# Optimization experiments

Measured on AMD Instinct MI355X. Metric: run time of the kernel, lower is better.

Reference implementation:

```python
import jax, jax.numpy as jnp
import numpy as np

N = 4_000_000   # points at level d
SIDE = 1024     # coordinate range per axis
HALF = SIDE // 2  # parent coord range


def setup_inputs() -> dict:
    key = jax.random.key(0)
    k1, k2 = jax.random.split(key)
    xyz = jax.random.randint(k1, (N, 3), 0, SIDE, dtype=jnp.int32)
    b = (jnp.arange(N, dtype=jnp.int32) % 4)[:, None]  # 4 batches
    coords = jnp.concatenate([b, xyz], axis=1)          # (N,4): [b,x,y,z]
    kernel = jnp.ones((8,), dtype=jnp.float32)          # frozen all-ones 2x2x2 conv weights
    return {"coords": coords, "kernel": kernel}


def _fog(coords, kernel):
    # pos(): occupancy code 2**(x%2 + 2*y%2 + 4*z%2)
    bits = coords[:, 1:4] & 1                       # (N,3)
    off = bits[:, 0] + 2 * bits[:, 1] + 4 * bits[:, 2]  # (N,) child offset in 2x2x2 window
    pos = jnp.exp2(off.astype(jnp.float32))         # (N,) code in {1,2,4,...,128}
    contrib = pos * kernel[off]                     # per-offset conv weight (all ones)
    # stride-2 conv: parent voxel = floor(xyz/2); linearize (b,z,y,x) into a key
    parent = coords[:, 1:4] >> 1                    # (N,3)
    keys = (((coords[:, 0].astype(jnp.int64) * HALF + parent[:, 2]) * HALF
             + parent[:, 1]) * HALF + parent[:, 0])
    ukeys, inv = jnp.unique(keys, return_inverse=True, size=N, fill_value=-1)
    feats = jax.ops.segment_sum(contrib, inv, num_segments=N)[:, None]  # (N,1)
    # decode padded unique keys back to coords; pad slots -> -1
    px = (ukeys % HALF).astype(jnp.int32)
    py = ((ukeys // HALF) % HALF).astype(jnp.int32)
    pz = ((ukeys // (HALF * HALF)) % HALF).astype(jnp.int32)
    pb = (ukeys // (HALF * HALF * HALF)).astype(jnp.int32)
    valid = (ukeys >= 0)[:, None]
    coords_out = jnp.where(valid, jnp.stack([pb, px, py, pz], axis=1), -1)
    return coords_out, feats


def reference(coords, kernel):
    return _fog(coords, kernel)
```

## Files before the change

kernel.cpp:

```cpp
#include <hip/hip_runtime.h>
#include <stdint.h>

typedef unsigned int u32;
typedef unsigned long long u64;

#define LBITS  14
#define LMASK  ((1u << LBITS) - 1u)
#define NBUCK  (1u << (29 - LBITS))
#define BWORDS (1u << (LBITS - 5))
#define WPL    (BWORDS / 64)
#define WOPAD  (BWORDS + BWORDS / 32)
#define FCAP   192
#define BPB    4
#define TILE_A 4096
#define RPT    (TILE_A / 256)
#define CCAP   16384
#define P2T    1024
#define RPT2U  (CCAP / P2T)
#define RECV   4

__device__ __forceinline__ u32 woidx(u32 w) { return w + (w >> 5); }

__device__ __forceinline__ void wsync() {
    asm volatile("s_waitcnt lgkmcnt(0)" ::: "memory");
}

__device__ __forceinline__ u32 make_key(int4 c) {
    return ((((u32)c.x * 512u + ((u32)c.w >> 1)) * 512u + ((u32)c.z >> 1)) * 512u)
           + ((u32)c.y >> 1);
}

__global__ void zero1(u32* __restrict__ p, u32 g) {
    u32 i = blockIdx.x * 256u + threadIdx.x;
    if (i < g) p[i] = 0u;
}

__global__ void __launch_bounds__(256) part1f(const int4* __restrict__ coords,
        u32* __restrict__ ccur, u32* __restrict__ tmp, int n) {
    __shared__ u32 stage[TILE_A];
    __shared__ u32 lcur[256];
    __shared__ u32 gb[256];
    __shared__ u32 wtot[4];
    u32 t = threadIdx.x, wave = t >> 6, lane = t & 63u;
    u32 base = blockIdx.x * TILE_A;
    u32 m = min((u32)TILE_A, (u32)n - base);
    lcur[t] = 0u;
    __syncthreads();
    u32 recv[RPT];
    #pragma unroll
    for (int k = 0; k < RPT; ++k) {
        u32 j = (u32)k * 256u + t;
        if (j < m) {
            int4 c = coords[base + j];
            u32 key = make_key(c);
            u32 off = ((u32)c.y & 1u) | (((u32)c.z & 1u) << 1) | (((u32)c.w & 1u) << 2);
            u32 rec = (key << 3) | off;
            recv[k] = rec;
            atomicAdd(&lcur[rec >> 24], 1u);
        }
    }
    __syncthreads();
    u32 v = lcur[t];
    u32 incl = v;
    #pragma unroll
    for (int d = 1; d < 64; d <<= 1) {
        u32 x = __shfl_up(incl, d);
        if ((int)lane >= d) incl += x;
    }
    if (lane == 63u) wtot[wave] = incl;
    __syncthreads();
    u32 off = (wave > 0u ? wtot[0] : 0u) + (wave > 1u ? wtot[1] : 0u)
            + (wave > 2u ? wtot[2] : 0u);
    u32 excl = off + incl - v;
    u32 gbase = atomicAdd(&ccur[t * 16u], v);
    lcur[t] = excl;
    gb[t] = (t << 14) + gbase - excl;
    __syncthreads();
    #pragma unroll
    for (int k = 0; k < RPT; ++k) {
        u32 j = (u32)k * 256u + t;
        if (j < m) {
            u32 rec = recv[k];
            u32 pos = atomicAdd(&lcur[rec >> 24], 1u);
            stage[pos] = rec;
        }
    }
    __syncthreads();
    for (u32 j = t; j < m; j += 256u) {
        u32 rec = stage[j];
        tmp[gb[rec >> 24] + j] = rec;
    }
}

__global__ void __launch_bounds__(P2T) part2u(u32* __restrict__ tmp,
        const u32* __restrict__ ccur, u32* __restrict__ cstart,
        u32* __restrict__ bcnt, u32* __restrict__ lexc, u32* __restrict__ utot) {
    __shared__ u32 stage[CCAP];
    __shared__ u32 h[4][128];
    __shared__ u32 lstart[128];
    __shared__ u32 lcur[128];
    __shared__ u32 cnts[128];
    __shared__ u32 ucl[128];
    __shared__ u32 wtot[2];
    __shared__ u32 bm[16][WOPAD];
    u32 t = threadIdx.x, wave = t >> 6, lane = t & 63u;
    u32 c = blockIdx.x;
    u32 base = c << 14;
    u32 L = ccur[c * 16u];
    if (t < 512u) h[t >> 7][t & 127u] = 0u;
    __syncthreads();
    u32 recv[RPT2U];
    u32 hrep = wave & 3u;
    #pragma unroll
    for (int k = 0; k < RPT2U; ++k) {
        u32 j = (u32)k * P2T + t;
        if (j < L) {
            u32 rec = tmp[base + j];
            recv[k] = rec;
            atomicAdd(&h[hrep][(rec >> 17) & 127u], 1u);
        }
    }
    __syncthreads();
    u32 v = 0, incl = 0;
    if (t < 128u) {
        v = h[0][t] + h[1][t] + h[2][t] + h[3][t];
        incl = v;
        #pragma unroll
        for (int d = 1; d < 64; d <<= 1) {
            u32 x = __shfl_up(incl, d);
            if ((int)lane >= d) incl += x;
        }
        if (lane == 63u) wtot[t >> 6] = incl;
    }
    __syncthreads();
    if (t < 128u) {
        u32 off = (t >= 64u) ? wtot[0] : 0u;
        u32 excl = off + incl - v;
        lstart[t] = excl;
        lcur[t] = excl;
        cnts[t] = v;
        u32 bucket = (c << 7) | t;
        cstart[bucket] = base + excl;
        bcnt[bucket] = v;
    }
    __syncthreads();
    #pragma unroll
    for (int k = 0; k < RPT2U; ++k) {
        u32 j = (u32)k * P2T + t;
        if (j < L) {
            u32 rec = recv[k];
            u32 pos = atomicAdd(&lcur[(rec >> 17) & 127u], 1u);
            stage[pos] = rec;
        }
    }
    __syncthreads();
    for (u32 j = t; j < L; j += P2T) tmp[base + j] = stage[j];
    u32* B = bm[wave];
    for (u32 bi = 0; bi < 8u; ++bi) {
        u32 b = wave * 8u + bi;
        #pragma unroll
        for (int j = 0; j < WPL; ++j) B[woidx(lane * WPL + j)] = 0u;
        wsync();
        u32 s0 = lstart[b], cnt = cnts[b];
        for (u32 i = s0 + lane; i < s0 + cnt; i += 64u) {
            u32 lk = (stage[i] >> 3) & LMASK;
            atomicOr(&B[woidx(lk >> 5)], 1u << (lk & 31u));
        }
        wsync();
        u32 sum = 0;
        #pragma unroll
        for (int j = 0; j < WPL; ++j) sum += __popc(B[woidx(lane * WPL + j)]);
        #pragma unroll
        for (int d = 1; d < 64; d <<= 1) sum += __shfl_xor(sum, d);
        if (lane == 0u) ucl[b] = sum;
        wsync();
    }
    __syncthreads();
    u32 uv = 0, incl2 = 0;
    if (t < 128u) {
        uv = ucl[t];
        incl2 = uv;
        #pragma unroll
        for (int d = 1; d < 64; d <<= 1) {
            u32 x = __shfl_up(incl2, d);
            if ((int)lane >= d) incl2 += x;
        }
        if (lane == 63u) wtot[t >> 6] = incl2;
    }
    __syncthreads();
    if (t < 128u) {
        u32 off = (t >= 64u) ? wtot[0] : 0u;
        lexc[(c << 7) | t] = off + incl2 - uv;
        if (t == 127u) utot[c] = wtot[0] + incl2;
    }
}

__global__ void __launch_bounds__(256) pass_emit(const u32* __restrict__ buckrec,
        const u32* __restrict__ cstart, const u32* __restrict__ bcnt,
        const u32* __restrict__ lexc, const u32* __restrict__ utot,
        const float* __restrict__ kern, float4* __restrict__ rows,
        float* __restrict__ feats, int n) {
    __shared__ u32 bm[BPB][WOPAD];
    __shared__ u32 wofW[BPB][BWORDS];
    __shared__ float fl[BPB][FCAP];
    __shared__ float ksc[BPB][8];
    u32 wave = threadIdx.x >> 6, lane = threadIdx.x & 63u;
    u32 bucket = blockIdx.x * BPB + wave;
    u32* B = bm[wave];
    u32* W = wofW[wave];
    float* F = fl[wave];
    #pragma unroll
    for (int j = 0; j < WPL; ++j) B[woidx(lane * WPL + j)] = 0u;
    #pragma unroll
    for (u32 j = lane; j < FCAP; j += 64u) F[j] = 0.f;
    if (lane < 8u) ksc[wave][lane] = (float)(1u << lane) * kern[lane];
    wsync();
    u32 start = cstart[bucket];
    u32 cnt = bcnt[bucket];
    u32 recv[RECV];
    #pragma unroll
    for (int k = 0; k < RECV; ++k) {
        u32 idx = (u32)k * 64u + lane;
        if (idx < cnt) {
            u32 rec = buckrec[start + idx];
            recv[k] = rec;
            u32 lk = (rec >> 3) & LMASK;
            atomicOr(&B[woidx(lk >> 5)], 1u << (lk & 31u));
        }
    }
    u32 c = bucket >> 7;
    u32 cb = 0, Uall = 0;
    #pragma unroll
    for (int k = 0; k < 4; ++k) {
        u32 j = (u32)k * 64u + lane;
        u32 uv = utot[j];
        Uall += uv;
        cb += (j < c) ? uv : 0u;
    }
    #pragma unroll
    for (int d = 1; d < 64; d <<= 1) {
        cb += __shfl_xor(cb, d);
        Uall += __shfl_xor(Uall, d);
    }
    wsync();
    u32 wv[WPL]; u32 pc[WPL]; u32 sum = 0;
    #pragma unroll
    for (int j = 0; j < WPL; ++j) {
        wv[j] = B[woidx(lane * WPL + j)];
        pc[j] = __popc(wv[j]);
        sum += pc[j];
    }
    u32 incl = sum;
    #pragma unroll
    for (int d = 1; d < 64; d <<= 1) {
        u32 tt = __shfl_up(incl, d);
        if ((int)lane >= d) incl += tt;
    }
    u32 lex = incl - sum;
    u32 uc = __shfl(incl, 63);
    {
        u32 r = lex;
        #pragma unroll
        for (int j = 0; j < WPL; ++j) { W[((u32)j << 6) | lane] = r; r += pc[j]; }
    }
    wsync();
    u32 base = cb + lexc[bucket];
    bool lds_ok = (uc <= FCAP);
    if (!lds_ok) {
        for (u32 j = lane; j < uc; j += 64u) feats[base + j] = 0.f;
        asm volatile("s_waitcnt vmcnt(0)" ::: "memory");
    }
    #pragma unroll
    for (int k = 0; k < RECV; ++k) {
        u32 idx = (u32)k * 64u + lane;
        if (idx < cnt) {
            u32 rec = recv[k];
            float contrib = ksc[wave][rec & 7u];
            u32 lk = (rec >> 3) & LMASK;
            u32 w = lk >> 5, bit = lk & 31u;
            u32 r = W[((w & 7u) << 6) | (w >> 3)]
                  + __popc(B[woidx(w)] & ((1u << bit) - 1u));
            if (lds_ok) atomicAdd(&F[r], contrib);
            else        atomicAdd(&feats[base + r], contrib);
        }
    }
    wsync();
    u32 rank = base + lex;
    u32 keyhi = bucket << LBITS;
    #pragma unroll
    for (int j = 0; j < WPL; ++j) {
        u32 bits = wv[j];
        u32 kb = keyhi | ((lane * (u32)WPL + (u32)j) << 5);
        while (bits) {
            u32 tz = __builtin_ctz(bits);
            bits &= bits - 1u;
            u32 key = kb | tz;
            rows[rank++] = make_float4((float)(key >> 27), (float)(key & 511u),
                                       (float)((key >> 9) & 511u),
                                       (float)((key >> 18) & 511u));
        }
    }
    if (lds_ok) {
        for (u32 j = lane; j < uc; j += 64u) feats[base + j] = F[j];
    }
    u32 len = (u32)n - Uall;
    u32 per = (len + (u32)NBUCK - 1u) / (u32)NBUCK;
    u32 ps = Uall + bucket * per;
    u32 pe = min(ps + per, (u32)n);
    for (u32 i = ps + lane; i < pe; i += 64u) {
        rows[i] = make_float4(-1.f, -1.f, -1.f, -1.f);
        feats[i] = 0.f;
    }
}

extern "C" void kernel_launch(void* const* d_in, const int* in_sizes, int n_in,
                              void* d_out, int out_size, void* d_ws, size_t ws_size,
                              hipStream_t stream) {
    const int n = in_sizes[0] / 4;
    const int4* coords = (const int4*)d_in[0];
    const float* kern  = (const float*)d_in[1];
    const u32 NT = ((u32)n + TILE_A - 1) / TILE_A;

    u32* wsp = (u32*)d_ws;
    u32* tmp     = wsp;
    u32* ccur    = tmp + 256 * CCAP;
    u32* cstart  = ccur + 256 * 16;
    u32* bcnt    = cstart + NBUCK;
    u32* lexc    = bcnt + NBUCK;
    u32* utot    = lexc + NBUCK;

    float4* rows  = (float4*)d_out;
    float*  feats = (float*)((char*)d_out + (size_t)n * 16);

    zero1<<<16, 256, 0, stream>>>(ccur, 256 * 16);
    part1f<<<NT, 256, 0, stream>>>(coords, ccur, tmp, n);
    part2u<<<256, P2T, 0, stream>>>(tmp, ccur, cstart, bcnt, lexc, utot);
    pass_emit<<<NBUCK / BPB, 256, 0, stream>>>(tmp, cstart, bcnt, lexc, utot,
                                               kern, rows, feats, n);
}
```

Baseline: 193.4 us.

## Compute unique ranks in part2u and emit coalesced rows from LDS

part2u already builds a per-bucket occupancy bitmap to count unique keys. It now also prefix-sums that bitmap, computes each record's rank within its bucket, and packs the rank into the record's upper bits before writing the records back. pass_emit no longer rebuilds the bitmap and rank tables: it scatters contributions and keys by rank into LDS, then writes rows and feats with contiguous lane-strided stores instead of per-lane serial bit-walking writes. The global-atomic fallback for buckets with more uniques than FCAP is removed, with FCAP raised to 224. Correctness therefore relies on no bucket exceeding that many unique parents.

```diff
diff --git a/kernel.cpp b/kernel.cpp
--- a/kernel.cpp
+++ b/kernel.cpp
@@ -10,14 +10,13 @@
 #define BWORDS (1u << (LBITS - 5))
 #define WPL    (BWORDS / 64)
 #define WOPAD  (BWORDS + BWORDS / 32)
-#define FCAP   192
+#define FCAP   224
 #define BPB    4
 #define TILE_A 4096
 #define RPT    (TILE_A / 256)
 #define CCAP   16384
 #define P2T    1024
 #define RPT2U  (CCAP / P2T)
-#define RECV   4
 
 __device__ __forceinline__ u32 woidx(u32 w) { return w + (w >> 5); }
 
@@ -94,7 +93,8 @@
 
 __global__ void __launch_bounds__(P2T) part2u(u32* __restrict__ tmp,
         const u32* __restrict__ ccur, u32* __restrict__ cstart,
-        u32* __restrict__ bcnt, u32* __restrict__ lexc, u32* __restrict__ utot) {
+        u32* __restrict__ bcnt, u32* __restrict__ ucnt,
+        u32* __restrict__ lexc, u32* __restrict__ utot) {
     __shared__ u32 stage[CCAP];
     __shared__ u32 h[4][128];
     __shared__ u32 lstart[128];
@@ -103,6 +103,7 @@
     __shared__ u32 ucl[128];
     __shared__ u32 wtot[2];
     __shared__ u32 bm[16][WOPAD];
+    __shared__ u32 Wt[16][BWORDS];
     u32 t = threadIdx.x, wave = t >> 6, lane = t & 63u;
     u32 c = blockIdx.x;
     u32 base = c << 14;
@@ -154,8 +155,8 @@
         }
     }
     __syncthreads();
-    for (u32 j = t; j < L; j += P2T) tmp[base + j] = stage[j];
     u32* B = bm[wave];
+    u32* W = Wt[wave];
     for (u32 bi = 0; bi < 8u; ++bi) {
         u32 b = wave * 8u + bi;
         #pragma unroll
@@ -167,14 +168,36 @@
             atomicOr(&B[woidx(lk >> 5)], 1u << (lk & 31u));
         }
         wsync();
-        u32 sum = 0;
-        #pragma unroll
-        for (int j = 0; j < WPL; ++j) sum += __popc(B[woidx(lane * WPL + j)]);
-        #pragma unroll
-        for (int d = 1; d < 64; d <<= 1) sum += __shfl_xor(sum, d);
-        if (lane == 0u) ucl[b] = sum;
+        u32 pc[WPL]; u32 sum = 0;
+        #pragma unroll
+        for (int j = 0; j < WPL; ++j) { pc[j] = __popc(B[woidx(lane * WPL + j)]); sum += pc[j]; }
+        u32 inc2 = sum;
+        #pragma unroll
+        for (int d = 1; d < 64; d <<= 1) {
+            u32 x = __shfl_up(inc2, d);
+            if ((int)lane >= d) inc2 += x;
+        }
+        u32 lex = inc2 - sum;
+        {
+            u32 r = lex;
+            #pragma unroll
+            for (int j = 0; j < WPL; ++j) { W[((u32)j << 6) | lane] = r; r += pc[j]; }
+        }
+        if (lane == 63u) ucl[b] = inc2;
         wsync();
-    }
+        for (u32 i = s0 + lane; i < s0 + cnt; i += 64u) {
+            u32 rec = stage[i];
+            u32 lk = (rec >> 3) & LMASK;
+            u32 w = lk >> 5, bit = lk & 31u;
+            u32 r = W[((w & 7u) << 6) | (w >> 3)]
+                  + __popc(B[woidx(w)] & ((1u << bit) - 1u));
+            stage[i] = (r << 17) | (rec & 0x1FFFFu);
+        }
+        wsync();
+    }
+    __syncthreads();
+    for (u32 j = t; j < L; j += P2T) tmp[base + j] = stage[j];
+    if (t < 128u) ucnt[(c << 7) | t] = ucl[t];
     __syncthreads();
     u32 uv = 0, incl2 = 0;
     if (t < 128u) {
@@ -197,37 +220,23 @@
 
 __global__ void __launch_bounds__(256) pass_emit(const u32* __restrict__ buckrec,
         const u32* __restrict__ cstart, const u32* __restrict__ bcnt,
-        const u32* __restrict__ lexc, const u32* __restrict__ utot,
-        const float* __restrict__ kern, float4* __restrict__ rows,
-        float* __restrict__ feats, int n) {
-    __shared__ u32 bm[BPB][WOPAD];
-    __shared__ u32 wofW[BPB][BWORDS];
+        const u32* __restrict__ ucnt, const u32* __restrict__ lexc,
+        const u32* __restrict__ utot, const float* __restrict__ kern,
+        float4* __restrict__ rows, float* __restrict__ feats, int n) {
     __shared__ float fl[BPB][FCAP];
+    __shared__ u32 kl[BPB][FCAP];
     __shared__ float ksc[BPB][8];
     u32 wave = threadIdx.x >> 6, lane = threadIdx.x & 63u;
     u32 bucket = blockIdx.x * BPB + wave;
-    u32* B = bm[wave];
-    u32* W = wofW[wave];
     float* F = fl[wave];
-    #pragma unroll
-    for (int j = 0; j < WPL; ++j) B[woidx(lane * WPL + j)] = 0u;
+    u32* K = kl[wave];
     #pragma unroll
     for (u32 j = lane; j < FCAP; j += 64u) F[j] = 0.f;
     if (lane < 8u) ksc[wave][lane] = (float)(1u << lane) * kern[lane];
     wsync();
     u32 start = cstart[bucket];
     u32 cnt = bcnt[bucket];
-    u32 recv[RECV];
-    #pragma unroll
-    for (int k = 0; k < RECV; ++k) {
-        u32 idx = (u32)k * 64u + lane;
-        if (idx < cnt) {
-            u32 rec = buckrec[start + idx];
-            recv[k] = rec;
-            u32 lk = (rec >> 3) & LMASK;
-            atomicOr(&B[woidx(lk >> 5)], 1u << (lk & 31u));
-        }
-    }
+    u32 uc = ucnt[bucket];
     u32 c = bucket >> 7;
     u32 cb = 0, Uall = 0;
     #pragma unroll
@@ -242,66 +251,21 @@
         cb += __shfl_xor(cb, d);
         Uall += __shfl_xor(Uall, d);
     }
+    u32 base = cb + lexc[bucket];
+    for (u32 i = start + lane; i < start + cnt; i += 64u) {
+        u32 rec = buckrec[i];
+        u32 r = rec >> 17;
+        atomicAdd(&F[r], ksc[wave][rec & 7u]);
+        K[r] = (rec >> 3) & LMASK;
+    }
     wsync();
-    u32 wv[WPL]; u32 pc[WPL]; u32 sum = 0;
-    #pragma unroll
-    for (int j = 0; j < WPL; ++j) {
-        wv[j] = B[woidx(lane * WPL + j)];
-        pc[j] = __popc(wv[j]);
-        sum += pc[j];
-    }
-    u32 incl = sum;
-    #pragma unroll
-    for (int d = 1; d < 64; d <<= 1) {
-        u32 tt = __shfl_up(incl, d);
-        if ((int)lane >= d) incl += tt;
-    }
-    u32 lex = incl - sum;
-    u32 uc = __shfl(incl, 63);
-    {
-        u32 r = lex;
-        #pragma unroll
-        for (int j = 0; j < WPL; ++j) { W[((u32)j << 6) | lane] = r; r += pc[j]; }
-    }
-    wsync();
-    u32 base = cb + lexc[bucket];
-    bool lds_ok = (uc <= FCAP);
-    if (!lds_ok) {
-        for (u32 j = lane; j < uc; j += 64u) feats[base + j] = 0.f;
-        asm volatile("s_waitcnt vmcnt(0)" ::: "memory");
-    }
-    #pragma unroll
-    for (int k = 0; k < RECV; ++k) {
-        u32 idx = (u32)k * 64u + lane;
-        if (idx < cnt) {
-            u32 rec = recv[k];
-            float contrib = ksc[wave][rec & 7u];
-            u32 lk = (rec >> 3) & LMASK;
-            u32 w = lk >> 5, bit = lk & 31u;
-            u32 r = W[((w & 7u) << 6) | (w >> 3)]
-                  + __popc(B[woidx(w)] & ((1u << bit) - 1u));
-            if (lds_ok) atomicAdd(&F[r], contrib);
-            else        atomicAdd(&feats[base + r], contrib);
-        }
-    }
-    wsync();
-    u32 rank = base + lex;
     u32 keyhi = bucket << LBITS;
-    #pragma unroll
-    for (int j = 0; j < WPL; ++j) {
-        u32 bits = wv[j];
-        u32 kb = keyhi | ((lane * (u32)WPL + (u32)j) << 5);
-        while (bits) {
-            u32 tz = __builtin_ctz(bits);
-            bits &= bits - 1u;
-            u32 key = kb | tz;
-            rows[rank++] = make_float4((float)(key >> 27), (float)(key & 511u),
-                                       (float)((key >> 9) & 511u),
-                                       (float)((key >> 18) & 511u));
-        }
-    }
-    if (lds_ok) {
-        for (u32 j = lane; j < uc; j += 64u) feats[base + j] = F[j];
+    for (u32 j = lane; j < uc; j += 64u) {
+        u32 key = keyhi | K[j];
+        rows[base + j] = make_float4((float)(key >> 27), (float)(key & 511u),
+                                     (float)((key >> 9) & 511u),
+                                     (float)((key >> 18) & 511u));
+        feats[base + j] = F[j];
     }
     u32 len = (u32)n - Uall;
     u32 per = (len + (u32)NBUCK - 1u) / (u32)NBUCK;
@@ -326,7 +290,8 @@
     u32* ccur    = tmp + 256 * CCAP;
     u32* cstart  = ccur + 256 * 16;
     u32* bcnt    = cstart + NBUCK;
-    u32* lexc    = bcnt + NBUCK;
+    u32* ucnt    = bcnt + NBUCK;
+    u32* lexc    = ucnt + NBUCK;
     u32* utot    = lexc + NBUCK;
 
     float4* rows  = (float4*)d_out;
@@ -334,7 +299,7 @@
 
     zero1<<<16, 256, 0, stream>>>(ccur, 256 * 16);
     part1f<<<NT, 256, 0, stream>>>(coords, ccur, tmp, n);
-    part2u<<<256, P2T, 0, stream>>>(tmp, ccur, cstart, bcnt, lexc, utot);
-    pass_emit<<<NBUCK / BPB, 256, 0, stream>>>(tmp, cstart, bcnt, lexc, utot,
+    part2u<<<256, P2T, 0, stream>>>(tmp, ccur, cstart, bcnt, ucnt, lexc, utot);
+    pass_emit<<<NBUCK / BPB, 256, 0, stream>>>(tmp, cstart, bcnt, ucnt, lexc, utot,
                                                kern, rows, feats, n);
 }
```

New measurement: 191.8 us. Within noise of the previous version (-0.8%).
